# Optimization experiments

Hardware: AMD Instinct MI355X
Metric: run time of the kernel (lower is better)

Reference implementation:

```python
import math
import jax, jax.numpy as jnp
import numpy as np

B, N, E, R = 1024, 200, 256, 256

def _layernorm(x, g, b, eps=1e-5):
    mu = x.mean(-1, keepdims=True)
    var = ((x - mu) ** 2).mean(-1, keepdims=True)
    return (x - mu) / jnp.sqrt(var + eps) * g + b

def setup_inputs() -> dict:
    key = jax.random.key(0)
    ks = jax.random.split(key, 16)
    d = {}
    d["e_emb"] = jax.random.normal(ks[0], (B, E), jnp.float32)
    d["nb_rel"] = jax.random.normal(ks[1], (B, N, R), jnp.float32)
    d["delta_t"] = jax.random.uniform(ks[2], (B, N), jnp.float32) * 10.0
    d["r_emb"] = jax.random.normal(ks[3], (B, R), jnp.float32)
    d["hist_mask"] = jax.random.randint(ks[4], (B, N), 0, 2).astype(bool)
    d["rel_w"] = jax.random.normal(ks[5], (E, R), jnp.float32) / math.sqrt(R)
    d["log_tau1"] = jnp.asarray(1.0, jnp.float32)
    d["log_tau2"] = jnp.asarray(2.5, jnp.float32)
    d["sharpness"] = jnp.asarray(1.5, jnp.float32)
    d["log_gamma"] = jnp.asarray(-2.0, jnp.float32)
    d["attn_w"] = jax.random.normal(ks[6], (3, E, E), jnp.float32) / math.sqrt(E)
    d["sp_w"] = jax.random.normal(ks[7], (3, E, 6 * E), jnp.float32) / math.sqrt(6 * E)
    d["sp_b"] = jnp.zeros((3, E), jnp.float32)
    d["ln_g"] = jnp.ones((3, E), jnp.float32)
    d["ln_b"] = jnp.zeros((3, E), jnp.float32)
    d["csq_w"] = jax.random.normal(ks[8], (E, R), jnp.float32) / math.sqrt(R)
    d["csq_b"] = jnp.zeros((E,), jnp.float32)
    d["csl_w"] = jax.random.normal(ks[9], (3, E), jnp.float32) / math.sqrt(E)
    d["csl_b"] = jnp.zeros((3,), jnp.float32)
    d["on_g"] = jnp.ones((E,), jnp.float32)
    d["on_b"] = jnp.zeros((E,), jnp.float32)
    return d

def _pna_one_scale(msgs, mask, e_emb, q_key, attn_w, sp_w, sp_b, ln_g, ln_b):
    # msgs: [B,N,E], mask: [B,N] bool, e_emb: [B,E], q_key: [B,E]
    valid_f = mask[..., None].astype(msgs.dtype)
    n_valid = jnp.maximum(mask.astype(msgs.dtype).sum(1, keepdims=True), 1.0)  # [B,1]
    msgs_v = msgs * valid_f
    mean_v = msgs_v.sum(1) / n_valid
    max_v = msgs_v.max(1)
    min_v = jnp.clip(jnp.where(mask[..., None], msgs, 10000.0).min(1), -10000.0, 10000.0)
    sq_m = (jnp.clip(msgs_v, -10.0, 10.0) ** 2).sum(1) / n_valid
    std_v = jnp.sqrt(jnp.maximum(sq_m - mean_v ** 2, 1e-6))
    q_proj = q_key @ attn_w.T  # [B,E]
    attn_raw = jnp.einsum('bne,be->bn', msgs, q_proj) / math.sqrt(msgs.shape[-1])
    attn_raw = jnp.where(mask, attn_raw, -10000.0)
    all_invalid = ~mask.any(1, keepdims=True)  # [B,1]
    attn_raw = jnp.where(all_invalid, 0.0, attn_raw)
    attn_p = jax.nn.softmax(attn_raw, axis=-1)
    attn_v = jnp.einsum('bn,bne->be', attn_p, msgs)
    feats = jnp.concatenate([mean_v, max_v, min_v, std_v, attn_v, e_emb], axis=-1)  # [B,6E]
    h = feats @ sp_w.T + sp_b
    h = _layernorm(h, ln_g, ln_b)
    return jax.nn.gelu(h, approximate=False)  # dropout = identity (eval mode)

def reference(e_emb, nb_rel, delta_t, r_emb, hist_mask, rel_w, log_tau1, log_tau2,
              sharpness, log_gamma, attn_w, sp_w, sp_b, ln_g, ln_b,
              csq_w, csq_b, csl_w, csl_b, on_g, on_b):
    msgs = jnp.einsum('bnr,er->bne', nb_rel, rel_w)
    gamma = jnp.exp(log_gamma)
    decay = jnp.exp(-gamma * jnp.maximum(delta_t, 0.0))
    msgs_dec = msgs * decay[..., None]
    tau1 = jnp.exp(log_tau1)
    tau2 = jnp.exp(log_tau2) + tau1
    sharp = jnp.clip(sharpness, 0.1, 5.0)
    w_fine = jax.nn.sigmoid(-sharp * (delta_t - tau1))
    w_coarse = jax.nn.sigmoid(sharp * (delta_t - tau2))
    w_mid = jnp.maximum(1.0 - w_fine - w_coarse, 0.0)
    scale_w = jnp.stack([w_fine, w_mid, w_coarse])  # [3,B,N]
    m_scales = msgs_dec[None] * scale_w[..., None]  # [3,B,N,E]
    q_key = r_emb @ rel_w.T  # [B,E]
    pna_v = jax.vmap(_pna_one_scale, in_axes=(0, None, None, None, 0, 0, 0, 0, 0))
    scales = pna_v(m_scales, hist_mask, e_emb, q_key, attn_w, sp_w, sp_b, ln_g, ln_b)  # [3,B,E]
    sq = r_emb @ csq_w.T + csq_b  # [B,E]
    logits = sq @ csl_w.T + csl_b  # [B,3]
    weights = jax.nn.softmax(logits, axis=-1)
    out = jnp.einsum('bs,sbe->be', weights, scales)
    return _layernorm(out, on_g, on_b)  # drop = identity (eval)
```

## Files before the change

kernel.cpp:

```cpp
#include <hip/hip_runtime.h>
#include <hip/hip_bf16.h>
#include <math.h>

#define B_   1024
#define N_   200
#define NR_  208
#define NT_  13
#define E_   256
#define R_   256
#define K6_  1536

typedef __attribute__((ext_vector_type(8))) short bf16x8;
typedef __attribute__((ext_vector_type(4))) float f32x4;

__device__ __forceinline__ unsigned short f2bf(float f) {
  unsigned int u = __float_as_uint(f);
  u += 0x7fffu + ((u >> 16) & 1u);
  return (unsigned short)(u >> 16);
}

__device__ __forceinline__ unsigned int pk_bf(float lo, float hi) {
  float2 t; t.x = lo; t.y = hi;
  __hip_bfloat162 h = __float22bfloat162_rn(t);
  unsigned int u;
  __builtin_memcpy(&u, &h, 4);
  return u;
}

__device__ __forceinline__ float gelu_exact(float x) {
  return 0.5f * x * (1.f + erff(x * 0.70710678118654752f));
}

__global__ __launch_bounds__(256) void k_cast(
    const float* __restrict__ rel_w, const float* __restrict__ sp_w,
    const float* __restrict__ csq_w, const float* __restrict__ attn_w,
    unsigned short* __restrict__ rwf, unsigned short* __restrict__ spwf,
    float* __restrict__ rwT, float* __restrict__ cwT, float* __restrict__ awT) {
  int o = blockIdx.x * 256 + threadIdx.x;
  if (o < 65536) {
    int j = o & 7, r16 = (o >> 3) & 15, quad = (o >> 7) & 3, ks = (o >> 9) & 7, et = o >> 12;
    rwf[o] = f2bf(rel_w[(size_t)(et * 16 + r16) * 256 + ks * 32 + quad * 8 + j]);
    return;
  }
  o -= 65536;
  if (o < 1179648) {
    int j = o & 7, r16 = (o >> 3) & 15, quad = (o >> 7) & 3, ks = (o >> 9) & 7;
    int rest = o >> 12;
    int kc = rest % 6, se = rest / 6;
    int et = se & 15, s = se >> 4;
    spwf[o] = f2bf(sp_w[(size_t)(s * 256 + et * 16 + r16) * 1536 + kc * 256 + ks * 32 + quad * 8 + j]);
    return;
  }
  o -= 1179648;
  if (o < 65536) { int r = o >> 8, e = o & 255; rwT[o] = rel_w[(size_t)e * 256 + r]; return; }
  o -= 65536;
  if (o < 65536) { int r = o >> 8, e = o & 255; cwT[o] = csq_w[(size_t)e * 256 + r]; return; }
  o -= 65536;
  if (o < 196608) {
    int s = o >> 16, rem = o & 65535, ep = rem >> 8, e = rem & 255;
    awT[o] = attn_w[((size_t)s * 256 + e) * 256 + ep];
  }
}

__global__ __launch_bounds__(256) void k_prep1(
    const float* __restrict__ r_emb, const float* __restrict__ rwT,
    const float* __restrict__ cwT, const float* __restrict__ csq_b,
    const float* __restrict__ csl_w, const float* __restrict__ csl_b,
    float* __restrict__ qk_ws, float* __restrict__ wts) {
  __shared__ __align__(16) float re[2][256];
  __shared__ float sqs[2][256];
  __shared__ float red[2][3][4];
  int b0 = blockIdx.x * 2;
  int tid = threadIdx.x, lane = tid & 63, wave = tid >> 6;
  int e = tid;
#pragma unroll
  for (int i = 0; i < 2; ++i)
    re[i][tid] = r_emb[(size_t)(b0 + i) * 256 + tid];
  __syncthreads();
  float qkv[2] = {0.f, 0.f}, sv[2] = {0.f, 0.f};
  for (int g = 0; g < 64; ++g) {
    float4 x0 = ((const float4*)re[0])[g];
    float4 x1 = ((const float4*)re[1])[g];
#pragma unroll
    for (int k = 0; k < 4; ++k) {
      int r = g * 4 + k;
      float w = rwT[(size_t)r * 256 + e];
      float c = cwT[(size_t)r * 256 + e];
      float xa = (k == 0) ? x0.x : (k == 1) ? x0.y : (k == 2) ? x0.z : x0.w;
      float xb = (k == 0) ? x1.x : (k == 1) ? x1.y : (k == 2) ? x1.z : x1.w;
      qkv[0] = fmaf(w, xa, qkv[0]); qkv[1] = fmaf(w, xb, qkv[1]);
      sv[0]  = fmaf(c, xa, sv[0]);  sv[1]  = fmaf(c, xb, sv[1]);
    }
  }
  float cb = csq_b[e];
#pragma unroll
  for (int i = 0; i < 2; ++i) {
    qk_ws[(size_t)(b0 + i) * 256 + e] = qkv[i];
    sqs[i][e] = sv[i] + cb;
  }
  __syncthreads();
#pragma unroll
  for (int i = 0; i < 2; ++i)
#pragma unroll
    for (int k = 0; k < 3; ++k) {
      float v = sqs[i][tid] * csl_w[k * 256 + tid];
#pragma unroll
      for (int o = 32; o >= 1; o >>= 1) v += __shfl_xor(v, o, 64);
      if (lane == 0) red[i][k][wave] = v;
    }
  __syncthreads();
  if (tid < 2) {
    int i = tid;
    float l[3];
#pragma unroll
    for (int k = 0; k < 3; ++k)
      l[k] = csl_b[k] + red[i][k][0] + red[i][k][1] + red[i][k][2] + red[i][k][3];
    float m = fmaxf(l[0], fmaxf(l[1], l[2]));
    float e0 = expf(l[0] - m), e1 = expf(l[1] - m), e2 = expf(l[2] - m);
    float inv = 1.f / (e0 + e1 + e2);
    wts[(b0 + i) * 4 + 0] = e0 * inv;
    wts[(b0 + i) * 4 + 1] = e1 * inv;
    wts[(b0 + i) * 4 + 2] = e2 * inv;
  }
}

__global__ __launch_bounds__(256) void k_prep2(
    const float* __restrict__ qk_ws, const float* __restrict__ awT,
    float* __restrict__ qp_ws) {
  __shared__ __align__(16) float qk[2][256];
  int b0 = blockIdx.x * 2;
  int tid = threadIdx.x;
  int e = tid;
#pragma unroll
  for (int i = 0; i < 2; ++i)
    qk[i][tid] = qk_ws[(size_t)(b0 + i) * 256 + tid];
  __syncthreads();
  float qpv[3][2];
#pragma unroll
  for (int s = 0; s < 3; ++s) { qpv[s][0] = 0.f; qpv[s][1] = 0.f; }
  for (int g = 0; g < 64; ++g) {
    float4 q0 = ((const float4*)qk[0])[g];
    float4 q1 = ((const float4*)qk[1])[g];
#pragma unroll
    for (int k = 0; k < 4; ++k) {
      int ep = g * 4 + k;
      float xa = (k == 0) ? q0.x : (k == 1) ? q0.y : (k == 2) ? q0.z : q0.w;
      float xb = (k == 0) ? q1.x : (k == 1) ? q1.y : (k == 2) ? q1.z : q1.w;
#pragma unroll
      for (int s = 0; s < 3; ++s) {
        float w = awT[((size_t)s * 256 + ep) * 256 + e];
        qpv[s][0] = fmaf(w, xa, qpv[s][0]);
        qpv[s][1] = fmaf(w, xb, qpv[s][1]);
      }
    }
  }
#pragma unroll
  for (int i = 0; i < 2; ++i)
#pragma unroll
    for (int s = 0; s < 3; ++s)
      qp_ws[((size_t)(b0 + i) * 3 + s) * 256 + e] = qpv[s][i];
}

__global__ __launch_bounds__(256) void k_prep3(
    const float* __restrict__ qp_ws, const float* __restrict__ rel_w,
    unsigned short* __restrict__ t_bf) {
  __shared__ __align__(16) float qp[2][3][256];
  int b0 = blockIdx.x * 2;
  int tid = threadIdx.x;
  int r = tid;
  for (int j = tid; j < 2 * 3 * 256; j += 256)
    ((float*)qp)[j] = qp_ws[(size_t)b0 * 768 + j];
  __syncthreads();
  float tacc[3][2];
#pragma unroll
  for (int s = 0; s < 3; ++s) { tacc[s][0] = 0.f; tacc[s][1] = 0.f; }
  for (int e4 = 0; e4 < 64; ++e4) {
    float4 qv[3][2];
#pragma unroll
    for (int s = 0; s < 3; ++s) {
      qv[s][0] = ((const float4*)qp[0][s])[e4];
      qv[s][1] = ((const float4*)qp[1][s])[e4];
    }
#pragma unroll
    for (int j = 0; j < 4; ++j) {
      float w = rel_w[(size_t)(e4 * 4 + j) * 256 + r];
#pragma unroll
      for (int s = 0; s < 3; ++s) {
        float qa = (j == 0) ? qv[s][0].x : (j == 1) ? qv[s][0].y : (j == 2) ? qv[s][0].z : qv[s][0].w;
        float qb = (j == 0) ? qv[s][1].x : (j == 1) ? qv[s][1].y : (j == 2) ? qv[s][1].z : qv[s][1].w;
        tacc[s][0] = fmaf(qa, w, tacc[s][0]);
        tacc[s][1] = fmaf(qb, w, tacc[s][1]);
      }
    }
  }
#pragma unroll
  for (int i = 0; i < 2; ++i)
#pragma unroll
    for (int s = 0; s < 3; ++s)
      t_bf[((size_t)(b0 + i) * 3 + s) * 256 + r] = f2bf(tacc[s][i]);
}

__global__ __launch_bounds__(1024, 4) void k1_main(
    const float* __restrict__ nb_rel, const float* __restrict__ delta_t,
    const unsigned char* __restrict__ hm_raw, const float* __restrict__ e_emb,
    const float* __restrict__ p_lt1, const float* __restrict__ p_lt2,
    const float* __restrict__ p_sh, const float* __restrict__ p_lgm,
    const unsigned short* __restrict__ rwf, const unsigned short* __restrict__ t_bf,
    unsigned short* __restrict__ feats) {
  __shared__ __align__(16) struct {
    unsigned int a[NR_ * 132];
    float c[3][NR_];
    float p[3][NR_];
    float nmeta[NR_ * 12];
  } sm;
  int b = blockIdx.x;
  int tid = threadIdx.x;
  int lane = tid & 63, wave = tid >> 6;
  int row16 = lane & 15, quad = lane >> 4;

  int hasNZoff = 0, hasFP = 0;
  {
    unsigned char cc = hm_raw[tid];
    if ((tid & 3) != 0 && cc != 0) {
      hasNZoff = 1;
      if (cc == 0x3Fu || cc == 0x80u) hasFP = 1;
    }
  }
  int cntNZ = __syncthreads_count(hasNZoff);
  int cntFP = __syncthreads_count(hasFP);
  int mmode = (cntNZ == 0) ? 0 : (cntFP > 0 ? 2 : 1);

  float tau1 = __expf(p_lt1[0]);
  float tau2 = __expf(p_lt2[0]) + tau1;
  float sharp = fminf(fmaxf(p_sh[0], 0.1f), 5.0f);
  float gamma = __expf(p_lgm[0]);

  bool mk = false;
  if (tid < NR_) {
    float mf = 0.f, c0 = 0.f, c1 = 0.f, c2 = 0.f;
    if (tid < N_) {
      size_t mi = (size_t)b * N_ + tid;
      if (mmode == 0)      mk = ((const int*)hm_raw)[mi] != 0;
      else if (mmode == 1) mk = hm_raw[mi] != 0;
      else                 mk = ((const float*)hm_raw)[mi] != 0.f;
      float dt = delta_t[mi];
      mf = mk ? 1.f : 0.f;
      float decay = __expf(-gamma * fmaxf(dt, 0.f));
      float wf = 1.f / (1.f + __expf(sharp * (dt - tau1)));
      float wc = 1.f / (1.f + __expf(-sharp * (dt - tau2)));
      float wm = fmaxf(1.f - wf - wc, 0.f);
      c0 = decay * wf; c1 = decay * wm; c2 = decay * wc;
    }
    sm.c[0][tid] = c0; sm.c[1][tid] = c1; sm.c[2][tid] = c2;
    f32x4 w0, w1;
    w0[0] = mf * c0; w0[1] = mf * c1; w0[2] = mf * c2; w0[3] = mk ? 0.f : 1e4f;
    w1[0] = 0.f; w1[1] = 0.f; w1[2] = 0.f; w1[3] = mf;
    *(f32x4*)&sm.nmeta[tid * 12]     = w0;
    *(f32x4*)&sm.nmeta[tid * 12 + 4] = w1;
  }
  int cnt = __syncthreads_count(mk ? 1 : 0);
  float nvf = fmaxf((float)cnt, 1.f);
  bool allinv = (cnt == 0);

  {
    const float* src = nb_rel + (size_t)b * N_ * 256;
    float4 xs[NT_];
#pragma unroll
    for (int i = 0; i < NT_; ++i) {
      int n = i * 16 + wave;
      int gn = (n < N_) ? n : (N_ - 1);
      xs[i] = *(const float4*)(src + (size_t)gn * 256 + lane * 4);
    }
#pragma unroll
    for (int i = 0; i < NT_; ++i) {
      uint2 pk;
      pk.x = pk_bf(xs[i].x, xs[i].y);
      pk.y = pk_bf(xs[i].z, xs[i].w);
      *(uint2*)&sm.a[(i * 16 + wave) * 132 + lane * 2] = pk;
    }
  }
  __syncthreads();

  if (wave < NT_) {
    bf16x8 tfrag[8];
    {
      int sr = (row16 < 3) ? row16 : 0;
      const unsigned short* tb = t_bf + ((size_t)b * 3 + sr) * 256 + quad * 8;
      bf16x8 zer = {0, 0, 0, 0, 0, 0, 0, 0};
#pragma unroll
      for (int ks = 0; ks < 8; ++ks) {
        bf16x8 tv = *(const bf16x8*)(tb + ks * 32);
        tfrag[ks] = (row16 < 3) ? tv : zer;
      }
    }
    f32x4 acc;
#pragma unroll
    for (int cc = 0; cc < 4; ++cc) acc[cc] = 0.f;
#pragma unroll
    for (int ks = 0; ks < 8; ++ks) {
      bf16x8 af = *(const bf16x8*)&sm.a[(wave * 16 + row16) * 132 + ks * 16 + quad * 4];
      acc = __builtin_amdgcn_mfma_f32_16x16x32_bf16(af, tfrag[ks], acc, 0, 0, 0);
    }
    if (row16 < 3) {
#pragma unroll
      for (int rg = 0; rg < 4; ++rg) {
        int n = wave * 16 + quad * 4 + rg;
        float cw = sm.c[row16][n];
        float mf = sm.nmeta[n * 12 + 7];
        float l = cw * acc[rg] * 0.0625f;
        l = (mf > 0.5f) ? l : -1e4f;
        if (allinv) l = (n < N_) ? 0.f : -1e4f;
        sm.p[row16][n] = l;
      }
    }
  } else if (wave == NT_) {
    for (int i = lane; i < 256; i += 64) {
      unsigned short v = f2bf(e_emb[(size_t)b * 256 + i]);
      feats[((size_t)0 * B_ + b) * K6_ + 1280 + i] = v;
      feats[((size_t)1 * B_ + b) * K6_ + 1280 + i] = v;
      feats[((size_t)2 * B_ + b) * K6_ + 1280 + i] = v;
    }
  }

  bf16x8 bfr[8];
  {
#pragma unroll
    for (int ks = 0; ks < 8; ++ks)
      bfr[ks] = *(const bf16x8*)(rwf + ((((size_t)wave * 8 + ks) * 4 + quad) * 16 + row16) * 8);
  }
  __syncthreads();

  if (wave < 3) {
    int s = wave;
    float m = -1e30f;
    for (int n = lane; n < NR_; n += 64) m = fmaxf(m, sm.p[s][n]);
#pragma unroll
    for (int o = 32; o >= 1; o >>= 1) m = fmaxf(m, __shfl_xor(m, o, 64));
    float ssum = 0.f;
    for (int n = lane; n < NR_; n += 64) {
      float ev = __expf(sm.p[s][n] - m);
      sm.p[s][n] = ev;
      ssum += ev;
    }
#pragma unroll
    for (int o = 32; o >= 1; o >>= 1) ssum += __shfl_xor(ssum, o, 64);
    float inv = 1.f / ssum;
    for (int n = lane; n < NR_; n += 64)
      sm.nmeta[n * 12 + 4 + s] = sm.p[s][n] * inv * sm.c[s][n];
  }
  __syncthreads();

  float s_mean[3], s_mx[3], s_mn[3], s_sq[3], s_av[3];
#pragma unroll
  for (int s = 0; s < 3; ++s) {
    s_mean[s] = 0.f; s_mx[s] = -1e30f; s_mn[s] = 1e30f;
    s_sq[s] = 0.f; s_av[s] = 0.f;
  }

  for (int nt = 0; nt < NT_; ++nt) {
    f32x4 acc;
#pragma unroll
    for (int cc = 0; cc < 4; ++cc) acc[cc] = 0.f;
#pragma unroll
    for (int ks = 0; ks < 8; ++ks) {
      bf16x8 af = *(const bf16x8*)&sm.a[(nt * 16 + row16) * 132 + ks * 16 + quad * 4];
      acc = __builtin_amdgcn_mfma_f32_16x16x32_bf16(af, bfr[ks], acc, 0, 0, 0);
    }
    int nb = nt * 16 + quad * 4;
#pragma unroll
    for (int rg = 0; rg < 4; ++rg) {
      const float* nm = &sm.nmeta[(size_t)(nb + rg) * 12];
      f32x4 w0 = *(const f32x4*)nm;
      f32x4 w1 = *(const f32x4*)(nm + 4);
      float m = acc[rg];
#pragma unroll
      for (int s = 0; s < 3; ++s) {
        float vm = w0[s] * m;
        s_mean[s] += vm;
        s_mx[s] = fmaxf(s_mx[s], vm);
        s_mn[s] = fminf(s_mn[s], fmaf(w0[s], m, w0[3]));
        float cv = fminf(fmaxf(vm, -10.f), 10.f);
        s_sq[s] = fmaf(cv, cv, s_sq[s]);
        s_av[s] = fmaf(w1[s], m, s_av[s]);
      }
    }
  }

#pragma unroll
  for (int s = 0; s < 3; ++s) {
    float vmean = s_mean[s];
    vmean += __shfl_xor(vmean, 16, 64); vmean += __shfl_xor(vmean, 32, 64);
    float vmx = s_mx[s];
    vmx = fmaxf(vmx, __shfl_xor(vmx, 16, 64)); vmx = fmaxf(vmx, __shfl_xor(vmx, 32, 64));
    float vmn = s_mn[s];
    vmn = fminf(vmn, __shfl_xor(vmn, 16, 64)); vmn = fminf(vmn, __shfl_xor(vmn, 32, 64));
    float vsq = s_sq[s];
    vsq += __shfl_xor(vsq, 16, 64); vsq += __shfl_xor(vsq, 32, 64);
    float vav = s_av[s];
    vav += __shfl_xor(vav, 16, 64); vav += __shfl_xor(vav, 32, 64);
    if (lane < 16) {
      int e = wave * 16 + lane;
      size_t base = ((size_t)s * B_ + b) * K6_;
      float meanv = vmean / nvf;
      float stdv = sqrtf(fmaxf(vsq / nvf - meanv * meanv, 1e-6f));
      float mnv = fminf(fmaxf(vmn, -1e4f), 1e4f);
      feats[base + e] = f2bf(meanv);
      feats[base + 256 + e] = f2bf(vmx);
      feats[base + 512 + e] = f2bf(mnv);
      feats[base + 768 + e] = f2bf(stdv);
      feats[base + 1024 + e] = f2bf(vav);
    }
  }
}

__global__ __launch_bounds__(256) void k2_kernel(
    const unsigned short* __restrict__ feats, const unsigned short* __restrict__ spwf,
    const float* __restrict__ sp_b, float* __restrict__ hbuf) {
  __shared__ __align__(16) unsigned short A[16][1544];
  int id = blockIdx.x;
  int s = id >> 8;
  int rem = id & 255;
  int b0 = (rem >> 2) * 16;
  int e0 = (rem & 3) * 64;
  int tid = threadIdx.x, lane = tid & 63, wave = tid >> 6;
  int row16 = lane & 15, quad = lane >> 4;

  bf16x8 v[12];
#pragma unroll
  for (int t = 0; t < 12; ++t) {
    int j = tid + t * 256;
    int rw = j / 192, ck = j % 192;
    v[t] = *(const bf16x8*)(feats + ((size_t)s * B_ + b0 + rw) * K6_ + ck * 8);
  }
#pragma unroll
  for (int t = 0; t < 12; ++t) {
    int j = tid + t * 256;
    int rw = j / 192, ck = j % 192;
    *(bf16x8*)&A[rw][ck * 8] = v[t];
  }
  __syncthreads();

  int et = (e0 >> 4) + wave;
  const unsigned short* bp = spwf + (((size_t)s * 16 + et) * 6) * 4096;
  f32x4 acc;
#pragma unroll
  for (int cc = 0; cc < 4; ++cc) acc[cc] = 0.f;
#pragma unroll
  for (int kc = 0; kc < 6; ++kc) {
#pragma unroll
    for (int ks = 0; ks < 8; ++ks) {
      bf16x8 af = *(const bf16x8*)&A[row16][kc * 256 + ks * 32 + quad * 8];
      bf16x8 bf = *(const bf16x8*)(bp + ((size_t)(kc * 8 + ks) * 4 + quad) * 128 + row16 * 8);
      acc = __builtin_amdgcn_mfma_f32_16x16x32_bf16(af, bf, acc, 0, 0, 0);
    }
  }
  {
    int e = e0 + wave * 16 + row16;
    float bias = sp_b[s * 256 + e];
#pragma unroll
    for (int rg = 0; rg < 4; ++rg) {
      int rw = quad * 4 + rg;
      hbuf[((size_t)s * B_ + b0 + rw) * 256 + e] = acc[rg] + bias;
    }
  }
}

__global__ __launch_bounds__(256) void k3_kernel(
    const float* __restrict__ hbuf, const float* __restrict__ wts,
    const float* __restrict__ ln_g, const float* __restrict__ ln_b,
    const float* __restrict__ on_g, const float* __restrict__ on_b,
    float* __restrict__ out) {
  __shared__ float rs[4], rq[4];
  int b = blockIdx.x, tid = threadIdx.x, lane = tid & 63, wave = tid >> 6;
  float o = 0.f;
#pragma unroll
  for (int s = 0; s < 3; ++s) {
    float h = hbuf[((size_t)s * B_ + b) * 256 + tid];
    float sum = h, sq = h * h;
#pragma unroll
    for (int off = 32; off >= 1; off >>= 1) {
      sum += __shfl_xor(sum, off, 64);
      sq += __shfl_xor(sq, off, 64);
    }
    if (lane == 0) { rs[wave] = sum; rq[wave] = sq; }
    __syncthreads();
    float ts = rs[0] + rs[1] + rs[2] + rs[3];
    float tq = rq[0] + rq[1] + rq[2] + rq[3];
    __syncthreads();
    float mu = ts * (1.f / 256.f);
    float var = tq * (1.f / 256.f) - mu * mu;
    float rstd = rsqrtf(var + 1e-5f);
    float v = (h - mu) * rstd * ln_g[s * 256 + tid] + ln_b[s * 256 + tid];
    o += wts[b * 4 + s] * gelu_exact(v);
  }
  float sum = o, sq = o * o;
#pragma unroll
  for (int off = 32; off >= 1; off >>= 1) {
    sum += __shfl_xor(sum, off, 64);
    sq += __shfl_xor(sq, off, 64);
  }
  if (lane == 0) { rs[wave] = sum; rq[wave] = sq; }
  __syncthreads();
  float ts = rs[0] + rs[1] + rs[2] + rs[3];
  float tq = rq[0] + rq[1] + rq[2] + rq[3];
  float mu = ts * (1.f / 256.f);
  float var = tq * (1.f / 256.f) - mu * mu;
  float rstd = rsqrtf(var + 1e-5f);
  out[(size_t)b * 256 + tid] = (o - mu) * rstd * on_g[tid] + on_b[tid];
}

extern "C" void kernel_launch(void* const* d_in, const int* in_sizes, int n_in,
                              void* d_out, int out_size, void* d_ws, size_t ws_size,
                              hipStream_t stream) {
  const float* e_emb   = (const float*)d_in[0];
  const float* nb_rel  = (const float*)d_in[1];
  const float* delta_t = (const float*)d_in[2];
  const float* r_emb   = (const float*)d_in[3];
  const unsigned char* hist_mask = (const unsigned char*)d_in[4];
  const float* rel_w   = (const float*)d_in[5];
  const float* lt1     = (const float*)d_in[6];
  const float* lt2     = (const float*)d_in[7];
  const float* shp     = (const float*)d_in[8];
  const float* lgm     = (const float*)d_in[9];
  const float* attn_w  = (const float*)d_in[10];
  const float* sp_w    = (const float*)d_in[11];
  const float* sp_b    = (const float*)d_in[12];
  const float* ln_g    = (const float*)d_in[13];
  const float* ln_b    = (const float*)d_in[14];
  const float* csq_w   = (const float*)d_in[15];
  const float* csq_b   = (const float*)d_in[16];
  const float* csl_w   = (const float*)d_in[17];
  const float* csl_b   = (const float*)d_in[18];
  const float* on_g    = (const float*)d_in[19];
  const float* on_b    = (const float*)d_in[20];
  float* out = (float*)d_out;

  char* ws = (char*)d_ws;
  unsigned short* rwf   = (unsigned short*)(ws + 0);
  unsigned short* spwf  = (unsigned short*)(ws + 131072);
  unsigned short* t_bf  = (unsigned short*)(ws + 2490368);
  float* wts    = (float*)(ws + 4063232);
  unsigned short* feats = (unsigned short*)(ws + 4079616);
  float* hbuf   = (float*)(ws + 13516800);
  float* rwT    = (float*)(ws + 16662528);
  float* cwT    = (float*)(ws + 16924672);
  float* awT    = (float*)(ws + 17186816);

  float* qk_ws = (float*)feats;
  float* qp_ws = hbuf;

  hipLaunchKernelGGL(k_cast, dim3(6144), dim3(256), 0, stream, rel_w, sp_w, csq_w, attn_w,
                     rwf, spwf, rwT, cwT, awT);
  hipLaunchKernelGGL(k_prep1, dim3(512), dim3(256), 0, stream, r_emb, rwT, cwT,
                     csq_b, csl_w, csl_b, qk_ws, wts);
  hipLaunchKernelGGL(k_prep2, dim3(512), dim3(256), 0, stream, qk_ws, awT, qp_ws);
  hipLaunchKernelGGL(k_prep3, dim3(512), dim3(256), 0, stream, qp_ws, rel_w, t_bf);
  hipLaunchKernelGGL(k1_main, dim3(1024), dim3(1024), 0, stream, nb_rel, delta_t, hist_mask,
                     e_emb, lt1, lt2, shp, lgm, rwf, t_bf, feats);
  hipLaunchKernelGGL(k2_kernel, dim3(768), dim3(256), 0, stream, feats, spwf, sp_b, hbuf);
  hipLaunchKernelGGL(k3_kernel, dim3(1024), dim3(256), 0, stream, hbuf, wts, ln_g, ln_b,
                     on_g, on_b, out);
}
```

Measured before the change: 474.0 us.

## Process four batches per k1 block with register prefetch of next batch

k1_main now runs 256 persistent-style blocks, each looping over four batch rows. The next row's nb_rel tile, delta_t and mask are loaded into registers while the current row's softmax and stats run, and the rel_w fragments are loaded once per block instead of per row. The goal is to hide global load latency and amortise the fixed per-block setup. In exchange there are only 256 blocks for 256 CUs, one 1024-thread block per CU, and launch_bounds is lowered to one block per CU, which reduces occupancy and raises register pressure from holding the prefetch buffers.

```diff
diff --git a/kernel.cpp b/kernel.cpp
--- a/kernel.cpp
+++ b/kernel.cpp
@@ -200,7 +200,7 @@
       t_bf[((size_t)(b0 + i) * 3 + s) * 256 + r] = f2bf(tacc[s][i]);
 }
 
-__global__ __launch_bounds__(1024, 4) void k1_main(
+__global__ __launch_bounds__(1024, 1) void k1_main(
     const float* __restrict__ nb_rel, const float* __restrict__ delta_t,
     const unsigned char* __restrict__ hm_raw, const float* __restrict__ e_emb,
     const float* __restrict__ p_lt1, const float* __restrict__ p_lt2,
@@ -213,7 +213,7 @@
     float p[3][NR_];
     float nmeta[NR_ * 12];
   } sm;
-  int b = blockIdx.x;
+  int b0 = blockIdx.x * 4;
   int tid = threadIdx.x;
   int lane = tid & 63, wave = tid >> 6;
   int row16 = lane & 15, quad = lane >> 4;
@@ -235,42 +235,57 @@
   float sharp = fminf(fmaxf(p_sh[0], 0.1f), 5.0f);
   float gamma = __expf(p_lgm[0]);
 
-  bool mk = false;
-  if (tid < NR_) {
-    float mf = 0.f, c0 = 0.f, c1 = 0.f, c2 = 0.f;
-    if (tid < N_) {
-      size_t mi = (size_t)b * N_ + tid;
-      if (mmode == 0)      mk = ((const int*)hm_raw)[mi] != 0;
-      else if (mmode == 1) mk = hm_raw[mi] != 0;
-      else                 mk = ((const float*)hm_raw)[mi] != 0.f;
-      float dt = delta_t[mi];
-      mf = mk ? 1.f : 0.f;
-      float decay = __expf(-gamma * fmaxf(dt, 0.f));
-      float wf = 1.f / (1.f + __expf(sharp * (dt - tau1)));
-      float wc = 1.f / (1.f + __expf(-sharp * (dt - tau2)));
-      float wm = fmaxf(1.f - wf - wc, 0.f);
-      c0 = decay * wf; c1 = decay * wm; c2 = decay * wc;
-    }
-    sm.c[0][tid] = c0; sm.c[1][tid] = c1; sm.c[2][tid] = c2;
-    f32x4 w0, w1;
-    w0[0] = mf * c0; w0[1] = mf * c1; w0[2] = mf * c2; w0[3] = mk ? 0.f : 1e4f;
-    w1[0] = 0.f; w1[1] = 0.f; w1[2] = 0.f; w1[3] = mf;
-    *(f32x4*)&sm.nmeta[tid * 12]     = w0;
-    *(f32x4*)&sm.nmeta[tid * 12 + 4] = w1;
-  }
-  int cnt = __syncthreads_count(mk ? 1 : 0);
-  float nvf = fmaxf((float)cnt, 1.f);
-  bool allinv = (cnt == 0);
-
+  bf16x8 bfr[8];
+#pragma unroll
+  for (int ks = 0; ks < 8; ++ks)
+    bfr[ks] = *(const bf16x8*)(rwf + ((((size_t)wave * 8 + ks) * 4 + quad) * 16 + row16) * 8);
+
+  float dt_c = 0.f;
+  unsigned int mkw = 0u;
+  if (tid < N_) {
+    size_t mi = (size_t)b0 * N_ + tid;
+    dt_c = delta_t[mi];
+    mkw = (mmode == 1) ? (unsigned int)hm_raw[mi] : ((const unsigned int*)hm_raw)[mi];
+  }
+  float4 xs[NT_];
   {
-    const float* src = nb_rel + (size_t)b * N_ * 256;
-    float4 xs[NT_];
+    const float* src = nb_rel + (size_t)b0 * N_ * 256;
 #pragma unroll
     for (int i = 0; i < NT_; ++i) {
       int n = i * 16 + wave;
       int gn = (n < N_) ? n : (N_ - 1);
       xs[i] = *(const float4*)(src + (size_t)gn * 256 + lane * 4);
     }
+  }
+
+  for (int bi = 0; bi < 4; ++bi) {
+    int b = b0 + bi;
+    if (bi > 0) __syncthreads();
+
+    bool mk = false;
+    if (tid < NR_) {
+      float mf = 0.f, c0 = 0.f, c1 = 0.f, c2 = 0.f;
+      if (tid < N_) {
+        mk = (mmode == 2) ? (__uint_as_float(mkw) != 0.f) : (mkw != 0u);
+        float dt = dt_c;
+        mf = mk ? 1.f : 0.f;
+        float decay = __expf(-gamma * fmaxf(dt, 0.f));
+        float wf = 1.f / (1.f + __expf(sharp * (dt - tau1)));
+        float wc = 1.f / (1.f + __expf(-sharp * (dt - tau2)));
+        float wm = fmaxf(1.f - wf - wc, 0.f);
+        c0 = decay * wf; c1 = decay * wm; c2 = decay * wc;
+      }
+      sm.c[0][tid] = c0; sm.c[1][tid] = c1; sm.c[2][tid] = c2;
+      f32x4 w0, w1;
+      w0[0] = mf * c0; w0[1] = mf * c1; w0[2] = mf * c2; w0[3] = mk ? 0.f : 1e4f;
+      w1[0] = 0.f; w1[1] = 0.f; w1[2] = 0.f; w1[3] = mf;
+      *(f32x4*)&sm.nmeta[tid * 12]     = w0;
+      *(f32x4*)&sm.nmeta[tid * 12 + 4] = w1;
+    }
+    int cnt = __syncthreads_count(mk ? 1 : 0);
+    float nvf = fmaxf((float)cnt, 1.f);
+    bool allinv = (cnt == 0);
+
 #pragma unroll
     for (int i = 0; i < NT_; ++i) {
       uint2 pk;
@@ -278,137 +293,146 @@
       pk.y = pk_bf(xs[i].z, xs[i].w);
       *(uint2*)&sm.a[(i * 16 + wave) * 132 + lane * 2] = pk;
     }
-  }
-  __syncthreads();
-
-  if (wave < NT_) {
-    bf16x8 tfrag[8];
-    {
-      int sr = (row16 < 3) ? row16 : 0;
-      const unsigned short* tb = t_bf + ((size_t)b * 3 + sr) * 256 + quad * 8;
-      bf16x8 zer = {0, 0, 0, 0, 0, 0, 0, 0};
+    __syncthreads();
+
+    if (wave < NT_) {
+      bf16x8 tfrag[8];
+      {
+        int sr = (row16 < 3) ? row16 : 0;
+        const unsigned short* tb = t_bf + ((size_t)b * 3 + sr) * 256 + quad * 8;
+        bf16x8 zer = {0, 0, 0, 0, 0, 0, 0, 0};
+#pragma unroll
+        for (int ks = 0; ks < 8; ++ks) {
+          bf16x8 tv = *(const bf16x8*)(tb + ks * 32);
+          tfrag[ks] = (row16 < 3) ? tv : zer;
+        }
+      }
+      f32x4 acc;
+#pragma unroll
+      for (int cc = 0; cc < 4; ++cc) acc[cc] = 0.f;
 #pragma unroll
       for (int ks = 0; ks < 8; ++ks) {
-        bf16x8 tv = *(const bf16x8*)(tb + ks * 32);
-        tfrag[ks] = (row16 < 3) ? tv : zer;
-      }
-    }
-    f32x4 acc;
-#pragma unroll
-    for (int cc = 0; cc < 4; ++cc) acc[cc] = 0.f;
-#pragma unroll
-    for (int ks = 0; ks < 8; ++ks) {
-      bf16x8 af = *(const bf16x8*)&sm.a[(wave * 16 + row16) * 132 + ks * 16 + quad * 4];
-      acc = __builtin_amdgcn_mfma_f32_16x16x32_bf16(af, tfrag[ks], acc, 0, 0, 0);
-    }
-    if (row16 < 3) {
+        bf16x8 af = *(const bf16x8*)&sm.a[(wave * 16 + row16) * 132 + ks * 16 + quad * 4];
+        acc = __builtin_amdgcn_mfma_f32_16x16x32_bf16(af, tfrag[ks], acc, 0, 0, 0);
+      }
+      if (row16 < 3) {
+#pragma unroll
+        for (int rg = 0; rg < 4; ++rg) {
+          int n = wave * 16 + quad * 4 + rg;
+          float cw = sm.c[row16][n];
+          float mf = sm.nmeta[n * 12 + 7];
+          float l = cw * acc[rg] * 0.0625f;
+          l = (mf > 0.5f) ? l : -1e4f;
+          if (allinv) l = (n < N_) ? 0.f : -1e4f;
+          sm.p[row16][n] = l;
+        }
+      }
+    } else if (wave == NT_) {
+      for (int i = lane; i < 256; i += 64) {
+        unsigned short v = f2bf(e_emb[(size_t)b * 256 + i]);
+        feats[((size_t)0 * B_ + b) * K6_ + 1280 + i] = v;
+        feats[((size_t)1 * B_ + b) * K6_ + 1280 + i] = v;
+        feats[((size_t)2 * B_ + b) * K6_ + 1280 + i] = v;
+      }
+    }
+
+    if (bi < 3) {
+      int bn = b + 1;
+      if (tid < N_) {
+        size_t mi = (size_t)bn * N_ + tid;
+        dt_c = delta_t[mi];
+        mkw = (mmode == 1) ? (unsigned int)hm_raw[mi] : ((const unsigned int*)hm_raw)[mi];
+      }
+      const float* src = nb_rel + (size_t)bn * N_ * 256;
+#pragma unroll
+      for (int i = 0; i < NT_; ++i) {
+        int n = i * 16 + wave;
+        int gn = (n < N_) ? n : (N_ - 1);
+        xs[i] = *(const float4*)(src + (size_t)gn * 256 + lane * 4);
+      }
+    }
+    __syncthreads();
+
+    if (wave < 3) {
+      int s = wave;
+      float m = -1e30f;
+      for (int n = lane; n < NR_; n += 64) m = fmaxf(m, sm.p[s][n]);
+#pragma unroll
+      for (int o = 32; o >= 1; o >>= 1) m = fmaxf(m, __shfl_xor(m, o, 64));
+      float ssum = 0.f;
+      for (int n = lane; n < NR_; n += 64) {
+        float ev = __expf(sm.p[s][n] - m);
+        sm.p[s][n] = ev;
+        ssum += ev;
+      }
+#pragma unroll
+      for (int o = 32; o >= 1; o >>= 1) ssum += __shfl_xor(ssum, o, 64);
+      float inv = 1.f / ssum;
+      for (int n = lane; n < NR_; n += 64)
+        sm.nmeta[n * 12 + 4 + s] = sm.p[s][n] * inv * sm.c[s][n];
+    }
+    __syncthreads();
+
+    float s_mean[3], s_mx[3], s_mn[3], s_sq[3], s_av[3];
+#pragma unroll
+    for (int s = 0; s < 3; ++s) {
+      s_mean[s] = 0.f; s_mx[s] = -1e30f; s_mn[s] = 1e30f;
+      s_sq[s] = 0.f; s_av[s] = 0.f;
+    }
+
+    for (int nt = 0; nt < NT_; ++nt) {
+      f32x4 acc;
+#pragma unroll
+      for (int cc = 0; cc < 4; ++cc) acc[cc] = 0.f;
+#pragma unroll
+      for (int ks = 0; ks < 8; ++ks) {
+        bf16x8 af = *(const bf16x8*)&sm.a[(nt * 16 + row16) * 132 + ks * 16 + quad * 4];
+        acc = __builtin_amdgcn_mfma_f32_16x16x32_bf16(af, bfr[ks], acc, 0, 0, 0);
+      }
+      int nb = nt * 16 + quad * 4;
 #pragma unroll
       for (int rg = 0; rg < 4; ++rg) {
-        int n = wave * 16 + quad * 4 + rg;
-        float cw = sm.c[row16][n];
-        float mf = sm.nmeta[n * 12 + 7];
-        float l = cw * acc[rg] * 0.0625f;
-        l = (mf > 0.5f) ? l : -1e4f;
-        if (allinv) l = (n < N_) ? 0.f : -1e4f;
-        sm.p[row16][n] = l;
-      }
-    }
-  } else if (wave == NT_) {
-    for (int i = lane; i < 256; i += 64) {
-      unsigned short v = f2bf(e_emb[(size_t)b * 256 + i]);
-      feats[((size_t)0 * B_ + b) * K6_ + 1280 + i] = v;
-      feats[((size_t)1 * B_ + b) * K6_ + 1280 + i] = v;
-      feats[((size_t)2 * B_ + b) * K6_ + 1280 + i] = v;
-    }
-  }
-
-  bf16x8 bfr[8];
-  {
-#pragma unroll
-    for (int ks = 0; ks < 8; ++ks)
-      bfr[ks] = *(const bf16x8*)(rwf + ((((size_t)wave * 8 + ks) * 4 + quad) * 16 + row16) * 8);
-  }
-  __syncthreads();
-
-  if (wave < 3) {
-    int s = wave;
-    float m = -1e30f;
-    for (int n = lane; n < NR_; n += 64) m = fmaxf(m, sm.p[s][n]);
-#pragma unroll
-    for (int o = 32; o >= 1; o >>= 1) m = fmaxf(m, __shfl_xor(m, o, 64));
-    float ssum = 0.f;
-    for (int n = lane; n < NR_; n += 64) {
-      float ev = __expf(sm.p[s][n] - m);
-      sm.p[s][n] = ev;
-      ssum += ev;
-    }
-#pragma unroll
-    for (int o = 32; o >= 1; o >>= 1) ssum += __shfl_xor(ssum, o, 64);
-    float inv = 1.f / ssum;
-    for (int n = lane; n < NR_; n += 64)
-      sm.nmeta[n * 12 + 4 + s] = sm.p[s][n] * inv * sm.c[s][n];
-  }
-  __syncthreads();
-
-  float s_mean[3], s_mx[3], s_mn[3], s_sq[3], s_av[3];
-#pragma unroll
-  for (int s = 0; s < 3; ++s) {
-    s_mean[s] = 0.f; s_mx[s] = -1e30f; s_mn[s] = 1e30f;
-    s_sq[s] = 0.f; s_av[s] = 0.f;
-  }
-
-  for (int nt = 0; nt < NT_; ++nt) {
-    f32x4 acc;
-#pragma unroll
-    for (int cc = 0; cc < 4; ++cc) acc[cc] = 0.f;
-#pragma unroll
-    for (int ks = 0; ks < 8; ++ks) {
-      bf16x8 af = *(const bf16x8*)&sm.a[(nt * 16 + row16) * 132 + ks * 16 + quad * 4];
-      acc = __builtin_amdgcn_mfma_f32_16x16x32_bf16(af, bfr[ks], acc, 0, 0, 0);
-    }
-    int nb = nt * 16 + quad * 4;
-#pragma unroll
-    for (int rg = 0; rg < 4; ++rg) {
-      const float* nm = &sm.nmeta[(size_t)(nb + rg) * 12];
-      f32x4 w0 = *(const f32x4*)nm;
-      f32x4 w1 = *(const f32x4*)(nm + 4);
-      float m = acc[rg];
-#pragma unroll
-      for (int s = 0; s < 3; ++s) {
-        float vm = w0[s] * m;
-        s_mean[s] += vm;
-        s_mx[s] = fmaxf(s_mx[s], vm);
-        s_mn[s] = fminf(s_mn[s], fmaf(w0[s], m, w0[3]));
-        float cv = fminf(fmaxf(vm, -10.f), 10.f);
-        s_sq[s] = fmaf(cv, cv, s_sq[s]);
-        s_av[s] = fmaf(w1[s], m, s_av[s]);
-      }
-    }
-  }
-
-#pragma unroll
-  for (int s = 0; s < 3; ++s) {
-    float vmean = s_mean[s];
-    vmean += __shfl_xor(vmean, 16, 64); vmean += __shfl_xor(vmean, 32, 64);
-    float vmx = s_mx[s];
-    vmx = fmaxf(vmx, __shfl_xor(vmx, 16, 64)); vmx = fmaxf(vmx, __shfl_xor(vmx, 32, 64));
-    float vmn = s_mn[s];
-    vmn = fminf(vmn, __shfl_xor(vmn, 16, 64)); vmn = fminf(vmn, __shfl_xor(vmn, 32, 64));
-    float vsq = s_sq[s];
-    vsq += __shfl_xor(vsq, 16, 64); vsq += __shfl_xor(vsq, 32, 64);
-    float vav = s_av[s];
-    vav += __shfl_xor(vav, 16, 64); vav += __shfl_xor(vav, 32, 64);
-    if (lane < 16) {
-      int e = wave * 16 + lane;
-      size_t base = ((size_t)s * B_ + b) * K6_;
-      float meanv = vmean / nvf;
-      float stdv = sqrtf(fmaxf(vsq / nvf - meanv * meanv, 1e-6f));
-      float mnv = fminf(fmaxf(vmn, -1e4f), 1e4f);
-      feats[base + e] = f2bf(meanv);
-      feats[base + 256 + e] = f2bf(vmx);
-      feats[base + 512 + e] = f2bf(mnv);
-      feats[base + 768 + e] = f2bf(stdv);
-      feats[base + 1024 + e] = f2bf(vav);
+        const float* nm = &sm.nmeta[(size_t)(nb + rg) * 12];
+        f32x4 w0 = *(const f32x4*)nm;
+        f32x4 w1 = *(const f32x4*)(nm + 4);
+        float m = acc[rg];
+#pragma unroll
+        for (int s = 0; s < 3; ++s) {
+          float vm = w0[s] * m;
+          s_mean[s] += vm;
+          s_mx[s] = fmaxf(s_mx[s], vm);
+          s_mn[s] = fminf(s_mn[s], fmaf(w0[s], m, w0[3]));
+          float cv = fminf(fmaxf(vm, -10.f), 10.f);
+          s_sq[s] = fmaf(cv, cv, s_sq[s]);
+          s_av[s] = fmaf(w1[s], m, s_av[s]);
+        }
+      }
+    }
+
+#pragma unroll
+    for (int s = 0; s < 3; ++s) {
+      float vmean = s_mean[s];
+      vmean += __shfl_xor(vmean, 16, 64); vmean += __shfl_xor(vmean, 32, 64);
+      float vmx = s_mx[s];
+      vmx = fmaxf(vmx, __shfl_xor(vmx, 16, 64)); vmx = fmaxf(vmx, __shfl_xor(vmx, 32, 64));
+      float vmn = s_mn[s];
+      vmn = fminf(vmn, __shfl_xor(vmn, 16, 64)); vmn = fminf(vmn, __shfl_xor(vmn, 32, 64));
+      float vsq = s_sq[s];
+      vsq += __shfl_xor(vsq, 16, 64); vsq += __shfl_xor(vsq, 32, 64);
+      float vav = s_av[s];
+      vav += __shfl_xor(vav, 16, 64); vav += __shfl_xor(vav, 32, 64);
+      if (lane < 16) {
+        int e = wave * 16 + lane;
+        size_t base = ((size_t)s * B_ + b) * K6_;
+        float meanv = vmean / nvf;
+        float stdv = sqrtf(fmaxf(vsq / nvf - meanv * meanv, 1e-6f));
+        float mnv = fminf(fmaxf(vmn, -1e4f), 1e4f);
+        feats[base + e] = f2bf(meanv);
+        feats[base + 256 + e] = f2bf(vmx);
+        feats[base + 512 + e] = f2bf(mnv);
+        feats[base + 768 + e] = f2bf(stdv);
+        feats[base + 1024 + e] = f2bf(vav);
+      }
     }
   }
 }
@@ -555,7 +579,7 @@
                      csq_b, csl_w, csl_b, qk_ws, wts);
   hipLaunchKernelGGL(k_prep2, dim3(512), dim3(256), 0, stream, qk_ws, awT, qp_ws);
   hipLaunchKernelGGL(k_prep3, dim3(512), dim3(256), 0, stream, qp_ws, rel_w, t_bf);
-  hipLaunchKernelGGL(k1_main, dim3(1024), dim3(1024), 0, stream, nb_rel, delta_t, hist_mask,
+  hipLaunchKernelGGL(k1_main, dim3(256), dim3(1024), 0, stream, nb_rel, delta_t, hist_mask,
                      e_emb, lt1, lt2, shp, lgm, rwf, t_bf, feats);
   hipLaunchKernelGGL(k2_kernel, dim3(768), dim3(256), 0, stream, feats, spwf, sp_b, hbuf);
   hipLaunchKernelGGL(k3_kernel, dim3(1024), dim3(256), 0, stream, hbuf, wts, ln_g, ln_b,
```

Result: slower. 534.8 us (+12.8%).
